# Optimization experiments

Hardware: AMD Instinct MI355X
Metric: run time of the kernel (lower is better)

The kernel has to match this reference:

```python
import jax, jax.numpy as jnp
import numpy as np

ITEM_NUM = 100000
EMBED = 128
HIDDEN = 256
BETA = 0.5
B = 4096
H = 200

def setup_inputs() -> dict:
    key = jax.random.key(0)
    ks = jax.random.split(key, 7)
    history = jax.random.randint(ks[0], (B, H), 0, ITEM_NUM)
    target = jax.random.randint(ks[1], (B,), 0, ITEM_NUM)
    embed_history = jax.random.normal(ks[2], (ITEM_NUM, EMBED), dtype=jnp.float32) * 0.01
    embed_target = jax.random.normal(ks[3], (ITEM_NUM, EMBED), dtype=jnp.float32) * 0.01
    # nn.Linear default init: U(-1/sqrt(fan_in), 1/sqrt(fan_in)); biases zeroed by _init_weight_
    lim1 = 1.0 / np.sqrt(EMBED)
    W1 = jax.random.uniform(ks[4], (EMBED, HIDDEN), dtype=jnp.float32, minval=-lim1, maxval=lim1)
    b1 = jnp.zeros((HIDDEN,), dtype=jnp.float32)
    lim2 = 1.0 / np.sqrt(HIDDEN)
    w2 = jax.random.uniform(ks[5], (HIDDEN,), dtype=jnp.float32, minval=-lim2, maxval=lim2)
    return {"history": history, "target": target, "embed_history": embed_history,
            "embed_target": embed_target, "W1": W1, "b1": b1, "w2": w2}

def reference(history, target, embed_history, embed_target, W1, b1, w2):
    hist_e = embed_history[history]            # [B, H, d]
    tgt_e = embed_target[target][:, None, :]   # [B, 1, d]
    x = hist_e * tgt_e                          # [B, H, d]
    a = jnp.einsum('bhk,k->bh', jax.nn.relu(jnp.einsum('bhd,dk->bhk', x, W1) + b1), w2)  # [B, H]
    mask = (history != target[:, None]).astype(a.dtype)  # [B, H]
    exp_A = jnp.exp(a) * mask                  # [B, H]
    denom = jnp.sum(exp_A, axis=-1) ** BETA    # [B], beta-power normalization (not softmax)
    attn = exp_A / denom[:, None]              # [B, H]
    pred = jnp.einsum('bh,bhd,bd->b', attn, hist_e, tgt_e[:, 0, :])  # [B]
    return jax.nn.sigmoid(pred)
```

## Files before the change

### kernel.cpp

```cpp
#include <hip/hip_runtime.h>

#define B_SZ   4096
#define H_SZ   200
#define D_SZ   128
#define N_SZ   256
#define ROWS   (B_SZ * H_SZ)
#define BM     64
#define TPB    8
#define RPB    (BM * TPB)
#define NBLK   (ROWS / RPB)

typedef _Float16 f16;
typedef __attribute__((ext_vector_type(2))) _Float16 f16x2;
typedef __attribute__((ext_vector_type(8))) _Float16 f16x8;
typedef __attribute__((ext_vector_type(4))) float f32x4;

union H8 { f16x8 v; f16x2 p[4]; uint4 u; };

__device__ __forceinline__ f16x2 pkrtz(float a, float b) {
    return __builtin_bit_cast(f16x2, __builtin_amdgcn_cvt_pkrtz(a, b));
}

__global__ __launch_bounds__(256) void cvt_eh(const float* __restrict__ src,
                                              uint4* __restrict__ dst, int n8) {
    int i = blockIdx.x * 256 + threadIdx.x;
    if (i >= n8) return;
    const f32x4* p = (const f32x4*)src + (size_t)i * 2;
    f32x4 a = p[0], b = p[1];
    uint4 o;
    o.x = __builtin_bit_cast(unsigned, pkrtz(a[0], a[1]));
    o.y = __builtin_bit_cast(unsigned, pkrtz(a[2], a[3]));
    o.z = __builtin_bit_cast(unsigned, pkrtz(b[0], b[1]));
    o.w = __builtin_bit_cast(unsigned, pkrtz(b[2], b[3]));
    dst[i] = o;
}

__global__ __launch_bounds__(256) void cvt_w1(const float* __restrict__ src,
                                              f16* __restrict__ dst) {
    int i = blockIdx.x * 256 + threadIdx.x;
    int n = i >> 7, d = i & 127;
    dst[i] = (f16)(src[d * N_SZ + n] * 0.0625f);
}

__global__ __launch_bounds__(512, 4) void nais_main(
    const int* __restrict__ history, const int* __restrict__ target,
    const uint4* __restrict__ ehh, const float* __restrict__ et,
    const f16* __restrict__ w1t, const float* __restrict__ b1,
    const float* __restrict__ w2,
    float* __restrict__ a_out, float* __restrict__ dotd_out)
{
    __shared__ uint4 AbufV[2][BM * 256 / 16];
    __shared__ float apart[2][8][BM];
    __shared__ f16   tgt_h[4][D_SZ];
    __shared__ int   tgt_i[4];

    const int tid  = threadIdx.x;
    const int wid  = tid >> 6;
    const int lane = tid & 63;
    const int lo   = lane & 15;
    const int hi   = lane >> 4;
    const int row  = tid >> 3;
    const int seg  = tid & 7;
    const int blk  = blockIdx.x;
    const int b_base = (blk * RPB) / H_SZ;

    if (tid < 4) {
        int bb = b_base + tid;
        tgt_i[tid] = target[bb < B_SZ ? bb : (B_SZ - 1)];
    }
    __syncthreads();
    if (tid < 256) {
        const int r4 = tid >> 6, j = (tid & 63) * 2;
        const float* src = et + (size_t)tgt_i[r4] * D_SZ + j;
        ((f16x2*)tgt_h)[tid] = pkrtz(src[0] * 16.f, src[1] * 16.f);
    }

    f16x8 wfrag[4][2];
    #pragma unroll
    for (int ni = 0; ni < 2; ++ni) {
        int n = 32 * wid + 16 * ni + lo;
        #pragma unroll
        for (int ki = 0; ki < 4; ++ki)
            wfrag[ki][ni] = *(const f16x8*)(w1t + (size_t)n * D_SZ + 32 * ki + 8 * hi);
    }
    const int n0 = 32 * wid + 4 * hi;
    const f32x4 b1a = *(const f32x4*)(b1 + n0);
    const f32x4 b1b = *(const f32x4*)(b1 + n0 + 16);
    const f32x4 w2a = *(const f32x4*)(w2 + n0);
    const f32x4 w2b = *(const f32x4*)(w2 + n0 + 16);

    const int grow0 = blk * RPB + row;
    const int* hrow = history + grow0;
    int ih_cur = hrow[0];
    int ih_nxt = hrow[BM];
    uint4 hq0, hq1;
    {
        const uint4* p = ehh + (size_t)ih_cur * 16;
        hq0 = p[seg]; hq1 = p[8 + seg];
    }
    int b_loc = grow0 / H_SZ - b_base;
    int rem   = grow0 - (b_loc + b_base) * H_SZ;
    __syncthreads();

    for (int t = 0; t < TPB; ++t) {
        char* Ab = (char*)AbufV[t & 1];
        const int gr = grow0 + t * BM;

        {
            H8 h1, h2, t1, t2, x1, x2;
            h1.u = hq0; h2.u = hq1;
            t1.v = *(const f16x8*)&tgt_h[b_loc][8 * seg];
            t2.v = *(const f16x8*)&tgt_h[b_loc][64 + 8 * seg];
            x1.v = h1.v * t1.v;
            x2.v = h2.v * t2.v;
            float s = 0.f;
            #pragma unroll
            for (int j = 0; j < 4; ++j) {
                s = __builtin_amdgcn_fdot2(h1.p[j], t1.p[j], s, false);
                s = __builtin_amdgcn_fdot2(h2.p[j], t2.p[j], s, false);
            }
            s += __shfl_xor(s, 1);
            s += __shfl_xor(s, 2);
            s += __shfl_xor(s, 4);
            if (seg == 0) dotd_out[gr] = s * 0.0625f;
            const unsigned sw = (unsigned)((row & 7) << 4);
            char* rb = Ab + row * 256;
            *(uint4*)(rb + (((unsigned)(16 * seg)) ^ sw))          = x1.u;
            *(uint4*)(rb + (128u + (((unsigned)(16 * seg)) ^ sw))) = x2.u;
        }
        __syncthreads();

        if (t + 1 < TPB) {
            ih_cur = ih_nxt;
            if (t + 2 < TPB) ih_nxt = hrow[(t + 2) * BM];
            const uint4* p = ehh + (size_t)ih_cur * 16;
            hq0 = p[seg]; hq1 = p[8 + seg];
        }

        if (t > 0 && tid < BM) {
            const float* ap = &apart[(t - 1) & 1][0][tid];
            float a = ap[0];
            #pragma unroll
            for (int w = 1; w < 8; ++w) a += ap[w * BM];
            a_out[blk * RPB + (t - 1) * BM + tid] = a;
        }

        #pragma unroll
        for (int mi = 0; mi < 4; ++mi) {
            const int rr = 16 * mi + lo;
            const unsigned swr = (unsigned)((rr & 7) << 4);
            f16x8 af[4];
            #pragma unroll
            for (int ki = 0; ki < 4; ++ki) {
                unsigned off = ((unsigned)(64 * ki + 16 * hi)) ^ swr;
                af[ki] = *(const f16x8*)(Ab + rr * 256 + off);
            }
            f32x4 acc0 = b1a;
            f32x4 acc1 = b1b;
            __builtin_amdgcn_s_setprio(1);
            #pragma unroll
            for (int ki = 0; ki < 4; ++ki) {
                acc0 = __builtin_amdgcn_mfma_f32_16x16x32_f16(wfrag[ki][0], af[ki], acc0, 0, 0, 0);
                acc1 = __builtin_amdgcn_mfma_f32_16x16x32_f16(wfrag[ki][1], af[ki], acc1, 0, 0, 0);
            }
            __builtin_amdgcn_s_setprio(0);
            float v = fmaxf(acc0[0], 0.f) * w2a[0] + fmaxf(acc1[0], 0.f) * w2b[0];
            v += fmaxf(acc0[1], 0.f) * w2a[1] + fmaxf(acc1[1], 0.f) * w2b[1];
            v += fmaxf(acc0[2], 0.f) * w2a[2] + fmaxf(acc1[2], 0.f) * w2b[2];
            v += fmaxf(acc0[3], 0.f) * w2a[3] + fmaxf(acc1[3], 0.f) * w2b[3];
            v += __shfl_xor(v, 16);
            v += __shfl_xor(v, 32);
            if (lane < 16) apart[t & 1][wid][16 * mi + lane] = v;
        }

        rem += BM;
        if (rem >= H_SZ) { rem -= H_SZ; ++b_loc; }
    }
    __syncthreads();
    if (tid < BM) {
        const float* ap = &apart[(TPB - 1) & 1][0][tid];
        float a = ap[0];
        #pragma unroll
        for (int w = 1; w < 8; ++w) a += ap[w * BM];
        a_out[blk * RPB + (TPB - 1) * BM + tid] = a;
    }
}

__global__ __launch_bounds__(64) void nais_finish(
    const int* __restrict__ history, const int* __restrict__ target,
    const float* __restrict__ a_in, const float* __restrict__ dotd_in,
    float* __restrict__ out)
{
    const int b    = blockIdx.x;
    const int lane = threadIdx.x;
    const int tgt  = target[b];
    float s1 = 0.f, s2 = 0.f;
    for (int h = lane; h < H_SZ; h += 64) {
        int rg = b * H_SZ + h;
        float e = (history[rg] != tgt) ? __expf(a_in[rg]) : 0.f;
        s1 += e;
        s2 += e * dotd_in[rg];
    }
    #pragma unroll
    for (int o = 1; o < 64; o <<= 1) {
        s1 += __shfl_xor(s1, o);
        s2 += __shfl_xor(s2, o);
    }
    if (lane == 0) {
        float pred = s2 / sqrtf(s1);
        out[b] = 1.f / (1.f + __expf(-pred));
    }
}

extern "C" void kernel_launch(void* const* d_in, const int* in_sizes, int n_in,
                              void* d_out, int out_size, void* d_ws, size_t ws_size,
                              hipStream_t stream) {
    const int*   history = (const int*)d_in[0];
    const int*   target  = (const int*)d_in[1];
    const float* eh      = (const float*)d_in[2];
    const float* et      = (const float*)d_in[3];
    const float* W1      = (const float*)d_in[4];
    const float* b1      = (const float*)d_in[5];
    const float* w2      = (const float*)d_in[6];
    float* out = (float*)d_out;

    char* ws = (char*)d_ws;
    uint4* ehh = (uint4*)ws;
    f16*   w1t = (f16*)(ws + (size_t)100000 * D_SZ * 2);
    float* a_ws = (float*)(ws + (size_t)100000 * D_SZ * 2 + N_SZ * D_SZ * 2);
    float* dotd_ws = a_ws + ROWS;

    const int n8 = 100000 * D_SZ / 8;
    cvt_eh<<<(n8 + 255) / 256, 256, 0, stream>>>(eh, ehh, n8);
    cvt_w1<<<(N_SZ * D_SZ) / 256, 256, 0, stream>>>(W1, w1t);
    nais_main<<<NBLK, 512, 0, stream>>>(history, target, ehh, et, w1t, b1, w2, a_ws, dotd_ws);
    nais_finish<<<B_SZ, 64, 0, stream>>>(history, target, a_ws, dotd_ws, out);
}
```

Baseline: 98.76 us.

## Fuse masked exp and weighted-sum reduction into main kernel via atomics

The per-row attention logits and dot products are no longer written to global memory for a separate finish kernel. The main kernel now applies the mask and exp itself, reduces each 64-row tile per batch element with wave shuffles, and atomically adds partial sums into per-batch accumulators. A small sigmoid kernel finishes the job. This removes the round trip of about 6.5 MB of intermediate data and a launch, at the cost of extra shuffles, global atomics and a zeroing kernel.

```diff
diff --git a/kernel.cpp b/kernel.cpp
--- a/kernel.cpp
+++ b/kernel.cpp
@@ -42,17 +42,25 @@
     dst[i] = (f16)(src[d * N_SZ + n] * 0.0625f);
 }
 
+__global__ __launch_bounds__(256) void zero_acc(float* __restrict__ s1g,
+                                                float* __restrict__ s2g) {
+    int i = blockIdx.x * 256 + threadIdx.x;
+    if (i < B_SZ) { s1g[i] = 0.f; s2g[i] = 0.f; }
+}
+
 __global__ __launch_bounds__(512, 4) void nais_main(
     const int* __restrict__ history, const int* __restrict__ target,
     const uint4* __restrict__ ehh, const float* __restrict__ et,
     const f16* __restrict__ w1t, const float* __restrict__ b1,
     const float* __restrict__ w2,
-    float* __restrict__ a_out, float* __restrict__ dotd_out)
+    float* __restrict__ s1g, float* __restrict__ s2g)
 {
     __shared__ uint4 AbufV[2][BM * 256 / 16];
     __shared__ float apart[2][8][BM];
     __shared__ f16   tgt_h[4][D_SZ];
     __shared__ int   tgt_i[4];
+    __shared__ float dotd_lds[3][BM];
+    __shared__ float m_lds[3][BM];
 
     const int tid  = threadIdx.x;
     const int wid  = tid >> 6;
@@ -102,9 +110,31 @@
     int rem   = grow0 - (b_loc + b_base) * H_SZ;
     __syncthreads();
 
+    #define REDUCE(TT)                                                            \
+    {                                                                             \
+        const float* ap = &apart[(TT) & 1][0][tid];                               \
+        float a = ap[0];                                                          \
+        _Pragma("unroll")                                                         \
+        for (int w = 1; w < 8; ++w) a += ap[w * BM];                              \
+        const int slot = (TT) % 3;                                                \
+        float e   = m_lds[slot][tid] * __expf(a);                                 \
+        float s2t = e * dotd_lds[slot][tid];                                      \
+        const int b = (blk * RPB + (TT) * BM + tid) / H_SZ;                       \
+        const int blo = __shfl(b, 0);                                             \
+        const bool ishi = (b != blo);                                             \
+        float e_lo = ishi ? 0.f : e,  d_lo = ishi ? 0.f : s2t;                    \
+        float e_hi = ishi ? e : 0.f,  d_hi = ishi ? s2t : 0.f;                    \
+        _Pragma("unroll")                                                         \
+        for (int o = 1; o < 64; o <<= 1) {                                        \
+            e_lo += __shfl_xor(e_lo, o); d_lo += __shfl_xor(d_lo, o);             \
+            e_hi += __shfl_xor(e_hi, o); d_hi += __shfl_xor(d_hi, o);             \
+        }                                                                         \
+        if (tid == 0)          { atomicAdd(&s1g[blo], e_lo); atomicAdd(&s2g[blo], d_lo); } \
+        if (tid == 63 && ishi) { atomicAdd(&s1g[b],   e_hi); atomicAdd(&s2g[b],   d_hi); } \
+    }
+
     for (int t = 0; t < TPB; ++t) {
         char* Ab = (char*)AbufV[t & 1];
-        const int gr = grow0 + t * BM;
 
         {
             H8 h1, h2, t1, t2, x1, x2;
@@ -122,7 +152,10 @@
             s += __shfl_xor(s, 1);
             s += __shfl_xor(s, 2);
             s += __shfl_xor(s, 4);
-            if (seg == 0) dotd_out[gr] = s * 0.0625f;
+            if (seg == 0) {
+                dotd_lds[t % 3][row] = s;
+                m_lds[t % 3][row] = (ih_cur != tgt_i[b_loc]) ? 1.f : 0.f;
+            }
             const unsigned sw = (unsigned)((row & 7) << 4);
             char* rb = Ab + row * 256;
             *(uint4*)(rb + (((unsigned)(16 * seg)) ^ sw))          = x1.u;
@@ -137,13 +170,7 @@
             hq0 = p[seg]; hq1 = p[8 + seg];
         }
 
-        if (t > 0 && tid < BM) {
-            const float* ap = &apart[(t - 1) & 1][0][tid];
-            float a = ap[0];
-            #pragma unroll
-            for (int w = 1; w < 8; ++w) a += ap[w * BM];
-            a_out[blk * RPB + (t - 1) * BM + tid] = a;
-        }
+        if (t > 0 && tid < BM) REDUCE(t - 1)
 
         #pragma unroll
         for (int mi = 0; mi < 4; ++mi) {
@@ -177,39 +204,17 @@
         if (rem >= H_SZ) { rem -= H_SZ; ++b_loc; }
     }
     __syncthreads();
-    if (tid < BM) {
-        const float* ap = &apart[(TPB - 1) & 1][0][tid];
-        float a = ap[0];
-        #pragma unroll
-        for (int w = 1; w < 8; ++w) a += ap[w * BM];
-        a_out[blk * RPB + (TPB - 1) * BM + tid] = a;
-    }
-}
-
-__global__ __launch_bounds__(64) void nais_finish(
-    const int* __restrict__ history, const int* __restrict__ target,
-    const float* __restrict__ a_in, const float* __restrict__ dotd_in,
-    float* __restrict__ out)
-{
-    const int b    = blockIdx.x;
-    const int lane = threadIdx.x;
-    const int tgt  = target[b];
-    float s1 = 0.f, s2 = 0.f;
-    for (int h = lane; h < H_SZ; h += 64) {
-        int rg = b * H_SZ + h;
-        float e = (history[rg] != tgt) ? __expf(a_in[rg]) : 0.f;
-        s1 += e;
-        s2 += e * dotd_in[rg];
-    }
-    #pragma unroll
-    for (int o = 1; o < 64; o <<= 1) {
-        s1 += __shfl_xor(s1, o);
-        s2 += __shfl_xor(s2, o);
-    }
-    if (lane == 0) {
-        float pred = s2 / sqrtf(s1);
-        out[b] = 1.f / (1.f + __expf(-pred));
-    }
+    if (tid < BM) REDUCE(TPB - 1)
+    #undef REDUCE
+}
+
+__global__ __launch_bounds__(256) void nais_sig(const float* __restrict__ s1g,
+                                                const float* __restrict__ s2g,
+                                                float* __restrict__ out) {
+    int b = blockIdx.x * 256 + threadIdx.x;
+    if (b >= B_SZ) return;
+    float pred = 0.0625f * s2g[b] / sqrtf(s1g[b]);
+    out[b] = 1.f / (1.f + __expf(-pred));
 }
 
 extern "C" void kernel_launch(void* const* d_in, const int* in_sizes, int n_in,
@@ -227,12 +232,13 @@
     char* ws = (char*)d_ws;
     uint4* ehh = (uint4*)ws;
     f16*   w1t = (f16*)(ws + (size_t)100000 * D_SZ * 2);
-    float* a_ws = (float*)(ws + (size_t)100000 * D_SZ * 2 + N_SZ * D_SZ * 2);
-    float* dotd_ws = a_ws + ROWS;
+    float* s1g = (float*)(ws + (size_t)100000 * D_SZ * 2 + N_SZ * D_SZ * 2);
+    float* s2g = s1g + B_SZ;
 
     const int n8 = 100000 * D_SZ / 8;
     cvt_eh<<<(n8 + 255) / 256, 256, 0, stream>>>(eh, ehh, n8);
     cvt_w1<<<(N_SZ * D_SZ) / 256, 256, 0, stream>>>(W1, w1t);
-    nais_main<<<NBLK, 512, 0, stream>>>(history, target, ehh, et, w1t, b1, w2, a_ws, dotd_ws);
-    nais_finish<<<B_SZ, 64, 0, stream>>>(history, target, a_ws, dotd_ws, out);
-}
+    zero_acc<<<(B_SZ + 255) / 256, 256, 0, stream>>>(s1g, s2g);
+    nais_main<<<NBLK, 512, 0, stream>>>(history, target, ehh, et, w1t, b1, w2, s1g, s2g);
+    nais_sig<<<(B_SZ + 255) / 256, 256, 0, stream>>>(s1g, s2g, out);
+}
```

Result: slower. 105.0 us (+6.3%).
